# Kernel tuning notes

Hardware: AMD Instinct MI355X
Metric: run time of the kernel (lower is better)

The kernel has to match this reference:

```python
import jax, jax.numpy as jnp
import numpy as np

N_NODES = 50000
N_EDGES = 800000
D = 64


def setup_inputs() -> dict:
    key = jax.random.key(0)
    k = jax.random.split(key, 8)
    h = jax.random.normal(k[0], (N_NODES, D), dtype=jnp.float32)
    edge_src = jax.random.randint(k[1], (N_EDGES,), 0, N_NODES, dtype=jnp.int32)
    edge_dst = jax.random.randint(k[2], (N_EDGES,), 0, N_NODES, dtype=jnp.int32)
    # normalized adjacency weights (e.g. 1/deg style values in (0,1))
    edge_w = jax.random.uniform(k[3], (N_EDGES,), dtype=jnp.float32)
    W_self = jax.random.normal(k[4], (D, D), dtype=jnp.float32) / np.sqrt(D)
    b_self = jnp.zeros((D,), dtype=jnp.float32)
    W_neigh = jax.random.normal(k[5], (D, D), dtype=jnp.float32) / np.sqrt(D)
    b_neigh = jnp.zeros((D,), dtype=jnp.float32)
    return {
        "h": h,
        "edge_src": edge_src,
        "edge_dst": edge_dst,
        "edge_w": edge_w,
        "W_self": W_self,
        "b_self": b_self,
        "W_neigh": W_neigh,
        "b_neigh": b_neigh,
    }


def reference(h, edge_src, edge_dst, edge_w, W_self, b_self, W_neigh, b_neigh):
    # neigh = A_norm @ h : sparse COO matmul as weighted gather + segment-sum
    # messages: [E, D]
    msgs = edge_w[:, None] * h[edge_src]
    neigh = jax.ops.segment_sum(msgs, edge_dst, num_segments=N_NODES)  # [N, D]
    # out = lin_self(h) + lin_neigh(neigh), relu; dropout is a no-op in eval mode
    out = (h @ W_self.T + b_self) + (neigh @ W_neigh.T + b_neigh)
    return jax.nn.relu(out)
```

## Files before the change

kernel.cpp:

```cpp
#include <hip/hip_runtime.h>

#define N_NODES 50000
#define N_EDGES 800000
#define D 64

#define NPB 200
#define NB  250
#define CAP 4096
#define BT  512
#define EPT 4
#define CHUNK_E (BT * EPT)
#define NCHUNKS ((N_EDGES + CHUNK_E - 1) / CHUNK_E)
#define CT  1024

typedef unsigned short ushort_t;
typedef unsigned int   uint_t;

__device__ __forceinline__ ushort_t f2b(float f) {
    uint_t u = __float_as_uint(f);
    return (ushort_t)((u + 0x7FFFu + ((u >> 16) & 1u)) >> 16);
}
__device__ __forceinline__ float b2f(ushort_t b) {
    return __uint_as_float((uint_t)b << 16);
}


__global__ __launch_bounds__(256) void h2b_kernel(
    const float* __restrict__ h, ushort_t* __restrict__ hb,
    int* __restrict__ cursor)
{
    if (blockIdx.x == 0 && threadIdx.x < NB) cursor[threadIdx.x] = threadIdx.x * CAP;
    const int i = blockIdx.x * 256 + threadIdx.x;
    if (i >= N_NODES * D / 4) return;
    const float4 v = ((const float4*)h)[i];
    ushort4 o;
    o.x = f2b(v.x); o.y = f2b(v.y); o.z = f2b(v.z); o.w = f2b(v.w);
    ((ushort4*)hb)[i] = o;
}

__global__ __launch_bounds__(BT) void bin_kernel(
    const int* __restrict__ src, const int* __restrict__ dst,
    const float* __restrict__ w, int* __restrict__ cursor,
    int2* __restrict__ bedges)
{
    __shared__ int lh[NB];
    __shared__ int loff[NB];
    __shared__ int lcur[NB];
    __shared__ int gpos[NB];
    __shared__ int part[256];
    __shared__ int2 stage[CHUNK_E];
    __shared__ unsigned char sbk[CHUNK_E];

    const int t = threadIdx.x;
    for (int i = t; i < NB; i += BT) lh[i] = 0;
    __syncthreads();

    const int base = blockIdx.x * CHUNK_E;
    int   my_b[EPT];
    int   my_p[EPT];
    float my_w[EPT];
#pragma unroll
    for (int k = 0; k < EPT; ++k) {
        const int e = base + k * BT + t;
        if (e < N_EDGES) {
            const int d = dst[e];
            const int b = (unsigned)d / NPB;
            my_b[k] = b;
            my_p[k] = (src[e] << 8) | (d - b * NPB);
            my_w[k] = w[e];
            atomicAdd(&lh[b], 1);
        } else {
            my_b[k] = -1;
        }
    }
    __syncthreads();

    const int v = (t < NB) ? lh[t] : 0;
    if (t < 256) part[t] = v;
    __syncthreads();
    for (int off = 1; off < 256; off <<= 1) {
        int p = 0;
        if (t < 256 && t >= off) p = part[t - off];
        __syncthreads();
        if (t < 256) part[t] += p;
        __syncthreads();
    }
    if (t < NB) { loff[t] = part[t] - v; lcur[t] = part[t] - v; }
    __syncthreads();

#pragma unroll
    for (int k = 0; k < EPT; ++k) {
        if (my_b[k] >= 0) {
            const int p = atomicAdd(&lcur[my_b[k]], 1);
            stage[p] = make_int2(my_p[k], __float_as_int(my_w[k]));
            sbk[p] = (unsigned char)my_b[k];
        }
    }
    __syncthreads();

    if (t < NB && lh[t] > 0) gpos[t] = atomicAdd(&cursor[t], lh[t]);
    __syncthreads();

    const int tot = min(N_EDGES - base, CHUNK_E);
    for (int s = t; s < tot; s += BT) {
        const int b = sbk[s];
        bedges[gpos[b] + (s - loff[b])] = stage[s];
    }
}

__global__ __launch_bounds__(CT) void bucket_csr_kernel(
    const int* __restrict__ cursor, int2* __restrict__ edges,
    int2* __restrict__ offs2)
{
    __shared__ int  lcur[NPB];
    __shared__ int  part[256];
    __shared__ int2 stage[CAP];

    const int b   = blockIdx.x;
    const int t   = threadIdx.x;
    const int gb  = b * CAP;
    const int cnt = min(cursor[b] - gb, CAP);

    if (t < NPB) lcur[t] = 0;
    __syncthreads();
    for (int e = t; e < cnt; e += CT)
        atomicAdd(&lcur[edges[gb + e].x & 255], 1);
    __syncthreads();

    const int v = (t < NPB) ? lcur[t] : 0;
    if (t < 256) part[t] = v;
    __syncthreads();
    for (int off = 1; off < 256; off <<= 1) {
        int p = 0;
        if (t < 256 && t >= off) p = part[t - off];
        __syncthreads();
        if (t < 256) part[t] += p;
        __syncthreads();
    }
    if (t < NPB) {
        const int ex = part[t] - v;
        lcur[t] = ex;
        offs2[b * NPB + t] = make_int2(gb + ex, gb + ex + v);
    }
    __syncthreads();

    for (int e = t; e < cnt; e += CT) {
        const int2 r = edges[gb + e];
        const int p = atomicAdd(&lcur[r.x & 255], 1);
        stage[p] = make_int2(r.x >> 8, r.y);
    }
    __syncthreads();
    for (int s = t; s < cnt; s += CT)
        edges[gb + s] = stage[s];
}

__global__ __launch_bounds__(256) void gather_kernel(
    const ushort_t* __restrict__ hb, const int2* __restrict__ edges,
    const int2* __restrict__ offs2, ushort_t* __restrict__ neigh)
{
    const int node = (blockIdx.x * 256 + threadIdx.x) >> 6;
    const int lane = threadIdx.x & 63;
    if (node >= N_NODES) return;
    const int2 be = offs2[node];
    const int beg = be.x, end = be.y;
    float acc = 0.f;
    int e = beg;
    for (; e + 8 <= end; e += 8) {
        int2  r[8];
        float vv[8];
#pragma unroll
        for (int k = 0; k < 8; ++k) r[k] = edges[e + k];
#pragma unroll
        for (int k = 0; k < 8; ++k) vv[k] = b2f(hb[(size_t)r[k].x * D + lane]);
#pragma unroll
        for (int k = 0; k < 8; ++k) acc = fmaf(__int_as_float(r[k].y), vv[k], acc);
    }
    for (; e + 4 <= end; e += 4) {
        const int2 e0 = edges[e], e1 = edges[e + 1], e2 = edges[e + 2], e3 = edges[e + 3];
        const float v0 = b2f(hb[(size_t)e0.x * D + lane]);
        const float v1 = b2f(hb[(size_t)e1.x * D + lane]);
        const float v2 = b2f(hb[(size_t)e2.x * D + lane]);
        const float v3 = b2f(hb[(size_t)e3.x * D + lane]);
        acc = fmaf(__int_as_float(e0.y), v0, acc);
        acc = fmaf(__int_as_float(e1.y), v1, acc);
        acc = fmaf(__int_as_float(e2.y), v2, acc);
        acc = fmaf(__int_as_float(e3.y), v3, acc);
    }
    for (; e < end; ++e) {
        const int2 ed = edges[e];
        acc = fmaf(__int_as_float(ed.y), b2f(hb[(size_t)ed.x * D + lane]), acc);
    }
    neigh[(size_t)node * D + lane] = f2b(acc);
}

__device__ __forceinline__ float lane_bcast(float v, int l) {
    return __int_as_float(__builtin_amdgcn_readlane(__float_as_int(v), l));
}

__global__ __launch_bounds__(256, 2) void linear_bf_kernel(
    const ushort_t* __restrict__ hb, const ushort_t* __restrict__ neigh,
    const float* __restrict__ Ws, const float* __restrict__ bs,
    const float* __restrict__ Wn, const float* __restrict__ bn,
    float* __restrict__ out)
{
    const int lane   = threadIdx.x & 63;
    const int gwave  = (blockIdx.x * blockDim.x + threadIdx.x) >> 6;
    const int nwaves = (gridDim.x * blockDim.x) >> 6;

    float Wsr[D], Wnr[D];
#pragma unroll
    for (int k = 0; k < D; k += 4) {
        const float4 a = *(const float4*)&Ws[(size_t)lane * D + k];
        const float4 b = *(const float4*)&Wn[(size_t)lane * D + k];
        Wsr[k] = a.x; Wsr[k+1] = a.y; Wsr[k+2] = a.z; Wsr[k+3] = a.w;
        Wnr[k] = b.x; Wnr[k+1] = b.y; Wnr[k+2] = b.z; Wnr[k+3] = b.w;
    }
    const float bias = bs[lane] + bn[lane];

    for (int n = gwave; n < N_NODES; n += nwaves) {
        const float hv = b2f(hb[(size_t)n * D + lane]);
        const float nv = b2f(neigh[(size_t)n * D + lane]);
        float o = bias;
#pragma unroll
        for (int k = 0; k < D; ++k) {
            o = fmaf(lane_bcast(hv, k), Wsr[k], o);
            o = fmaf(lane_bcast(nv, k), Wnr[k], o);
        }
        out[(size_t)n * D + lane] = fmaxf(o, 0.f);
    }
}

__global__ __launch_bounds__(256) void sage_scatter(
    const float* __restrict__ h,
    const int* __restrict__ edge_src,
    const int* __restrict__ edge_dst,
    const float* __restrict__ edge_w,
    float* __restrict__ neigh)
{
    const long long tid = (long long)blockIdx.x * blockDim.x + threadIdx.x;
    const int e = (int)(tid >> 6);
    const int d = (int)(tid & 63);
    if (e >= N_EDGES) return;
    atomicAdd(&neigh[(long long)edge_dst[e] * D + d],
              edge_w[e] * h[(long long)edge_src[e] * D + d]);
}

__global__ __launch_bounds__(256, 2) void linear_f32_kernel(
    const float* __restrict__ h, const float* __restrict__ neigh,
    const float* __restrict__ Ws, const float* __restrict__ bs,
    const float* __restrict__ Wn, const float* __restrict__ bn,
    float* __restrict__ out)
{
    const int lane   = threadIdx.x & 63;
    const int gwave  = (blockIdx.x * blockDim.x + threadIdx.x) >> 6;
    const int nwaves = (gridDim.x * blockDim.x) >> 6;

    float Wsr[D], Wnr[D];
#pragma unroll
    for (int k = 0; k < D; k += 4) {
        const float4 a = *(const float4*)&Ws[(size_t)lane * D + k];
        const float4 b = *(const float4*)&Wn[(size_t)lane * D + k];
        Wsr[k] = a.x; Wsr[k+1] = a.y; Wsr[k+2] = a.z; Wsr[k+3] = a.w;
        Wnr[k] = b.x; Wnr[k+1] = b.y; Wnr[k+2] = b.z; Wnr[k+3] = b.w;
    }
    const float bias = bs[lane] + bn[lane];

    for (int n = gwave; n < N_NODES; n += nwaves) {
        const float hv = h[(size_t)n * D + lane];
        const float nv = neigh[(size_t)n * D + lane];
        float o = bias;
#pragma unroll
        for (int k = 0; k < D; ++k) {
            o = fmaf(lane_bcast(hv, k), Wsr[k], o);
            o = fmaf(lane_bcast(nv, k), Wnr[k], o);
        }
        out[(size_t)n * D + lane] = fmaxf(o, 0.f);
    }
}

extern "C" void kernel_launch(void* const* d_in, const int* in_sizes, int n_in,
                              void* d_out, int out_size, void* d_ws, size_t ws_size,
                              hipStream_t stream)
{
    const float* h        = (const float*)d_in[0];
    const int*   edge_src = (const int*)d_in[1];
    const int*   edge_dst = (const int*)d_in[2];
    const float* edge_w   = (const float*)d_in[3];
    const float* W_self   = (const float*)d_in[4];
    const float* b_self   = (const float*)d_in[5];
    const float* W_neigh  = (const float*)d_in[6];
    const float* b_neigh  = (const float*)d_in[7];
    float*       out      = (float*)d_out;

    int2*     edges  = (int2*)d_ws;
    int2*     offs2  = edges + (size_t)NB * CAP;
    ushort_t* hb     = (ushort_t*)(offs2 + N_NODES);
    ushort_t* neighb = hb + (size_t)N_NODES * D;
    int*      cursor = (int*)(neighb + (size_t)N_NODES * D);
    const size_t needed = (size_t)NB * CAP * 8 + (size_t)N_NODES * 8
                        + (size_t)N_NODES * D * 2 * 2 + NB * 4;

    if (ws_size >= needed) {
        h2b_kernel<<<(N_NODES * D / 4 + 255) / 256, 256, 0, stream>>>(h, hb, cursor);
        bin_kernel<<<NCHUNKS, BT, 0, stream>>>(edge_src, edge_dst, edge_w,
                                               cursor, edges);
        bucket_csr_kernel<<<NB, CT, 0, stream>>>(cursor, edges, offs2);
        gather_kernel<<<(N_NODES * 64 + 255) / 256, 256, 0, stream>>>(
            hb, edges, offs2, neighb);
        linear_bf_kernel<<<1024, 256, 0, stream>>>(hb, neighb, W_self, b_self,
                                                   W_neigh, b_neigh, out);
    } else {
        float* neigh_fb = (float*)d_ws;
        hipMemsetAsync(neigh_fb, 0, (size_t)N_NODES * D * sizeof(float), stream);
        const long long total = (long long)N_EDGES * 64;
        sage_scatter<<<(int)((total + 255) / 256), 256, 0, stream>>>(
            h, edge_src, edge_dst, edge_w, neigh_fb);
        linear_f32_kernel<<<1024, 256, 0, stream>>>(h, neigh_fb, W_self, b_self,
                                                    W_neigh, b_neigh, out);
    }
}
```

Baseline: 167.6 us.

## Fuse gather into linear kernel and merge bf16 conversion into binning

```diff
diff --git a/kernel.cpp b/kernel.cpp
--- a/kernel.cpp
+++ b/kernel.cpp
@@ -12,6 +12,7 @@
 #define CHUNK_E (BT * EPT)
 #define NCHUNKS ((N_EDGES + CHUNK_E - 1) / CHUNK_E)
 #define CT  1024
+#define GL_BLOCKS 768
 
 typedef unsigned short ushort_t;
 typedef unsigned int   uint_t;
@@ -23,26 +24,29 @@
 __device__ __forceinline__ float b2f(ushort_t b) {
     return __uint_as_float((uint_t)b << 16);
 }
-
-
-__global__ __launch_bounds__(256) void h2b_kernel(
-    const float* __restrict__ h, ushort_t* __restrict__ hb,
-    int* __restrict__ cursor)
-{
-    if (blockIdx.x == 0 && threadIdx.x < NB) cursor[threadIdx.x] = threadIdx.x * CAP;
-    const int i = blockIdx.x * 256 + threadIdx.x;
-    if (i >= N_NODES * D / 4) return;
-    const float4 v = ((const float4*)h)[i];
-    ushort4 o;
-    o.x = f2b(v.x); o.y = f2b(v.y); o.z = f2b(v.z); o.w = f2b(v.w);
-    ((ushort4*)hb)[i] = o;
-}
-
-__global__ __launch_bounds__(BT) void bin_kernel(
+__device__ __forceinline__ float lane_bcast(float v, int l) {
+    return __int_as_float(__builtin_amdgcn_readlane(__float_as_int(v), l));
+}
+
+
+__global__ __launch_bounds__(BT) void bin_h2b_kernel(
     const int* __restrict__ src, const int* __restrict__ dst,
     const float* __restrict__ w, int* __restrict__ cursor,
-    int2* __restrict__ bedges)
-{
+    int2* __restrict__ bedges,
+    const float* __restrict__ h, ushort_t* __restrict__ hb)
+{
+    if (blockIdx.x >= NCHUNKS) {
+        const int nb = gridDim.x - NCHUNKS;
+        for (int i = (blockIdx.x - NCHUNKS) * BT + threadIdx.x;
+             i < N_NODES * D / 4; i += nb * BT) {
+            const float4 v = ((const float4*)h)[i];
+            ushort4 o;
+            o.x = f2b(v.x); o.y = f2b(v.y); o.z = f2b(v.z); o.w = f2b(v.w);
+            ((ushort4*)hb)[i] = o;
+        }
+        return;
+    }
+
     __shared__ int lh[NB];
     __shared__ int loff[NB];
     __shared__ int lcur[NB];
@@ -98,7 +102,8 @@
     }
     __syncthreads();
 
-    if (t < NB && lh[t] > 0) gpos[t] = atomicAdd(&cursor[t], lh[t]);
+    if (t < NB && lh[t] > 0)
+        gpos[t] = t * CAP + atomicAdd(&cursor[t], lh[t]);
     __syncthreads();
 
     const int tot = min(N_EDGES - base, CHUNK_E);
@@ -119,7 +124,7 @@
     const int b   = blockIdx.x;
     const int t   = threadIdx.x;
     const int gb  = b * CAP;
-    const int cnt = min(cursor[b] - gb, CAP);
+    const int cnt = min(cursor[b], CAP);
 
     if (t < NPB) lcur[t] = 0;
     __syncthreads();
@@ -154,51 +159,9 @@
         edges[gb + s] = stage[s];
 }
 
-__global__ __launch_bounds__(256) void gather_kernel(
+__global__ __launch_bounds__(256) void gather_linear_kernel(
     const ushort_t* __restrict__ hb, const int2* __restrict__ edges,
-    const int2* __restrict__ offs2, ushort_t* __restrict__ neigh)
-{
-    const int node = (blockIdx.x * 256 + threadIdx.x) >> 6;
-    const int lane = threadIdx.x & 63;
-    if (node >= N_NODES) return;
-    const int2 be = offs2[node];
-    const int beg = be.x, end = be.y;
-    float acc = 0.f;
-    int e = beg;
-    for (; e + 8 <= end; e += 8) {
-        int2  r[8];
-        float vv[8];
-#pragma unroll
-        for (int k = 0; k < 8; ++k) r[k] = edges[e + k];
-#pragma unroll
-        for (int k = 0; k < 8; ++k) vv[k] = b2f(hb[(size_t)r[k].x * D + lane]);
-#pragma unroll
-        for (int k = 0; k < 8; ++k) acc = fmaf(__int_as_float(r[k].y), vv[k], acc);
-    }
-    for (; e + 4 <= end; e += 4) {
-        const int2 e0 = edges[e], e1 = edges[e + 1], e2 = edges[e + 2], e3 = edges[e + 3];
-        const float v0 = b2f(hb[(size_t)e0.x * D + lane]);
-        const float v1 = b2f(hb[(size_t)e1.x * D + lane]);
-        const float v2 = b2f(hb[(size_t)e2.x * D + lane]);
-        const float v3 = b2f(hb[(size_t)e3.x * D + lane]);
-        acc = fmaf(__int_as_float(e0.y), v0, acc);
-        acc = fmaf(__int_as_float(e1.y), v1, acc);
-        acc = fmaf(__int_as_float(e2.y), v2, acc);
-        acc = fmaf(__int_as_float(e3.y), v3, acc);
-    }
-    for (; e < end; ++e) {
-        const int2 ed = edges[e];
-        acc = fmaf(__int_as_float(ed.y), b2f(hb[(size_t)ed.x * D + lane]), acc);
-    }
-    neigh[(size_t)node * D + lane] = f2b(acc);
-}
-
-__device__ __forceinline__ float lane_bcast(float v, int l) {
-    return __int_as_float(__builtin_amdgcn_readlane(__float_as_int(v), l));
-}
-
-__global__ __launch_bounds__(256, 2) void linear_bf_kernel(
-    const ushort_t* __restrict__ hb, const ushort_t* __restrict__ neigh,
+    const int2* __restrict__ offs2,
     const float* __restrict__ Ws, const float* __restrict__ bs,
     const float* __restrict__ Wn, const float* __restrict__ bn,
     float* __restrict__ out)
@@ -207,24 +170,62 @@
     const int gwave  = (blockIdx.x * blockDim.x + threadIdx.x) >> 6;
     const int nwaves = (gridDim.x * blockDim.x) >> 6;
 
-    float Wsr[D], Wnr[D];
+    uint_t Wsp[D / 2], Wnp[D / 2];
 #pragma unroll
     for (int k = 0; k < D; k += 4) {
         const float4 a = *(const float4*)&Ws[(size_t)lane * D + k];
         const float4 b = *(const float4*)&Wn[(size_t)lane * D + k];
-        Wsr[k] = a.x; Wsr[k+1] = a.y; Wsr[k+2] = a.z; Wsr[k+3] = a.w;
-        Wnr[k] = b.x; Wnr[k+1] = b.y; Wnr[k+2] = b.z; Wnr[k+3] = b.w;
+        Wsp[k / 2]     = (uint_t)f2b(a.x) | ((uint_t)f2b(a.y) << 16);
+        Wsp[k / 2 + 1] = (uint_t)f2b(a.z) | ((uint_t)f2b(a.w) << 16);
+        Wnp[k / 2]     = (uint_t)f2b(b.x) | ((uint_t)f2b(b.y) << 16);
+        Wnp[k / 2 + 1] = (uint_t)f2b(b.z) | ((uint_t)f2b(b.w) << 16);
     }
     const float bias = bs[lane] + bn[lane];
 
     for (int n = gwave; n < N_NODES; n += nwaves) {
+        const int2 be = offs2[n];
+        const int beg = be.x, end = be.y;
+
+        float acc = 0.f;
+        int e = beg;
+        for (; e + 8 <= end; e += 8) {
+            int2  r[8];
+            float vv[8];
+#pragma unroll
+            for (int k = 0; k < 8; ++k) r[k] = edges[e + k];
+#pragma unroll
+            for (int k = 0; k < 8; ++k) vv[k] = b2f(hb[(size_t)r[k].x * D + lane]);
+#pragma unroll
+            for (int k = 0; k < 8; ++k) acc = fmaf(__int_as_float(r[k].y), vv[k], acc);
+        }
+        for (; e + 4 <= end; e += 4) {
+            const int2 e0 = edges[e], e1 = edges[e + 1], e2 = edges[e + 2], e3 = edges[e + 3];
+            const float v0 = b2f(hb[(size_t)e0.x * D + lane]);
+            const float v1 = b2f(hb[(size_t)e1.x * D + lane]);
+            const float v2 = b2f(hb[(size_t)e2.x * D + lane]);
+            const float v3 = b2f(hb[(size_t)e3.x * D + lane]);
+            acc = fmaf(__int_as_float(e0.y), v0, acc);
+            acc = fmaf(__int_as_float(e1.y), v1, acc);
+            acc = fmaf(__int_as_float(e2.y), v2, acc);
+            acc = fmaf(__int_as_float(e3.y), v3, acc);
+        }
+        for (; e < end; ++e) {
+            const int2 ed = edges[e];
+            acc = fmaf(__int_as_float(ed.y), b2f(hb[(size_t)ed.x * D + lane]), acc);
+        }
+
         const float hv = b2f(hb[(size_t)n * D + lane]);
-        const float nv = b2f(neigh[(size_t)n * D + lane]);
         float o = bias;
 #pragma unroll
-        for (int k = 0; k < D; ++k) {
-            o = fmaf(lane_bcast(hv, k), Wsr[k], o);
-            o = fmaf(lane_bcast(nv, k), Wnr[k], o);
+        for (int i = 0; i < D / 2; ++i) {
+            const float h0 = lane_bcast(hv, 2 * i);
+            const float h1 = lane_bcast(hv, 2 * i + 1);
+            const float n0 = lane_bcast(acc, 2 * i);
+            const float n1 = lane_bcast(acc, 2 * i + 1);
+            o = fmaf(h0, __uint_as_float(Wsp[i] << 16), o);
+            o = fmaf(h1, __uint_as_float(Wsp[i] & 0xFFFF0000u), o);
+            o = fmaf(n0, __uint_as_float(Wnp[i] << 16), o);
+            o = fmaf(n1, __uint_as_float(Wnp[i] & 0xFFFF0000u), o);
         }
         out[(size_t)n * D + lane] = fmaxf(o, 0.f);
     }
@@ -295,20 +296,17 @@
     int2*     edges  = (int2*)d_ws;
     int2*     offs2  = edges + (size_t)NB * CAP;
     ushort_t* hb     = (ushort_t*)(offs2 + N_NODES);
-    ushort_t* neighb = hb + (size_t)N_NODES * D;
-    int*      cursor = (int*)(neighb + (size_t)N_NODES * D);
+    int*      cursor = (int*)(hb + (size_t)N_NODES * D);
     const size_t needed = (size_t)NB * CAP * 8 + (size_t)N_NODES * 8
-                        + (size_t)N_NODES * D * 2 * 2 + NB * 4;
+                        + (size_t)N_NODES * D * 2 + NB * 4;
 
     if (ws_size >= needed) {
-        h2b_kernel<<<(N_NODES * D / 4 + 255) / 256, 256, 0, stream>>>(h, hb, cursor);
-        bin_kernel<<<NCHUNKS, BT, 0, stream>>>(edge_src, edge_dst, edge_w,
-                                               cursor, edges);
+        hipMemsetAsync(cursor, 0, NB * sizeof(int), stream);
+        bin_h2b_kernel<<<NCHUNKS * 2, BT, 0, stream>>>(
+            edge_src, edge_dst, edge_w, cursor, edges, h, hb);
         bucket_csr_kernel<<<NB, CT, 0, stream>>>(cursor, edges, offs2);
-        gather_kernel<<<(N_NODES * 64 + 255) / 256, 256, 0, stream>>>(
-            hb, edges, offs2, neighb);
-        linear_bf_kernel<<<1024, 256, 0, stream>>>(hb, neighb, W_self, b_self,
-                                                   W_neigh, b_neigh, out);
+        gather_linear_kernel<<<GL_BLOCKS, 256, 0, stream>>>(
+            hb, edges, offs2, W_self, b_self, W_neigh, b_neigh, out);
     } else {
         float* neigh_fb = (float*)d_ws;
         hipMemsetAsync(neigh_fb, 0, (size_t)N_NODES * D * sizeof(float), stream);
```

Measured after the change: 218.5 us. 1.3x slower.
